# Kernel optimization log

Measured on AMD Instinct MI355X. Metric: run time of the kernel, lower is better.

The kernel has to match this reference:

```python
import jax, jax.numpy as jnp
import numpy as np

KSIZE = 3   # patch kernel
NSIZE = 7   # search neighborhood
SCALE = 4   # downscale factor
ALPHA = 1


def _patches(x, k, pad_mode):
    # x: [b,c,h,w] -> [b, c*k*k, h, w], feature ordering channel-major
    # (matches torch.nn.functional.unfold ordering).
    if pad_mode == 'reflect':
        p = k // 2
        xp = jnp.pad(x, ((0, 0), (0, 0), (p, p), (p, p)), mode='reflect')
        return jax.lax.conv_general_dilated_patches(xp, (k, k), (1, 1), 'VALID')
    return jax.lax.conv_general_dilated_patches(x, (k, k), (1, 1), 'SAME')


def census(x):
    # UFlow-style soft census transform (the CensusTransform used in this repo):
    # grayscale*255, 3x3 zero-padded patches minus center, soft-sign normalize.
    gray = (0.299 * x[:, 0:1] + 0.587 * x[:, 1:2] + 0.114 * x[:, 2:3]) * 255.0
    p = _patches(gray, KSIZE, 'zero')          # [b, 9, h, w]
    t = p - gray
    return t / jnp.sqrt(0.81 + t * t)


def downsample(x):
    b, c, h, w = x.shape
    return jax.image.resize(x, (b, c, h // SCALE, w // SCALE), method='cubic')


def unfold_center(x):
    # _unfold(data, with_unfold=False): [b,c,h,w] -> [b, hw, c*k*k]
    x = downsample(x)
    b, c, h, w = x.shape
    p = _patches(x, KSIZE, 'reflect').reshape(b, c * KSIZE * KSIZE, h * w)
    return p.transpose(0, 2, 1)


def unfold_nbr(x):
    # _unfold(data, with_unfold=True): [b,c,h,w] -> [b, hw, n*n, c*k*k]
    x = downsample(x)
    b, c, h, w = x.shape
    d1 = _patches(x, KSIZE, 'reflect')          # [b, c*k*k, h, w]
    c1 = d1.shape[1]
    d2 = _patches(d1, NSIZE, 'reflect')         # [b, c1*n*n, h, w]
    d2 = d2.reshape(b, c1, NSIZE * NSIZE, h * w)
    return d2.transpose(0, 3, 2, 1)


def reference(pred, I):
    # --- census-space distance + argmin over 2*n*n candidates ---
    p_ct = unfold_center(census(pred))                       # [b, hw, 81]
    nbr_ct = jnp.concatenate(
        [unfold_nbr(census(I[:, 0])), unfold_nbr(census(I[:, 1]))], axis=2
    )                                                        # [b, hw, 2n^2, 81]
    # ||p - n||^2 expanded as p2 + n2 - 2 p.n (avoids the huge repeated diff)
    p2 = jnp.sum(p_ct * p_ct, axis=-1)                       # [b, hw]
    n2 = jnp.sum(nbr_ct * nbr_ct, axis=-1)                   # [b, hw, 2n^2]
    dis = p2[:, :, None] + n2 - 2.0 * jnp.einsum('bpc,bpnc->bpn', p_ct, nbr_ct)
    ind = jnp.argmin(dis, axis=2)                            # [b, hw]
    # --- gather matched raw patches and compute loss ---
    p = unfold_center(pred)                                  # [b, hw, 27]
    nbr = jnp.concatenate(
        [unfold_nbr(I[:, 0]), unfold_nbr(I[:, 1])], axis=2
    )                                                        # [b, hw, 2n^2, 27]
    matched = jnp.take_along_axis(nbr, ind[:, :, None, None], axis=2)[:, :, 0]
    return jnp.mean((p - matched) ** 2 * 0.5)


def setup_inputs() -> dict:
    key = jax.random.key(0)
    k1, k2 = jax.random.split(key)
    pred = jax.random.normal(k1, (2, 3, 384, 384), dtype=jnp.float32)
    I = jax.random.normal(k2, (2, 2, 3, 384, 384), dtype=jnp.float32)
    return {'pred': pred, 'I': I}
```

## Files before the change

kernel.cpp:

```cpp
#include <hip/hip_runtime.h>
#include <math.h>

#define FH 384
#define FW 384
#define DH 96
#define DW 96
#define NIMG 6
#define PLANE (DH * DW)
#define NPIX (2 * PLANE)

__device__ __forceinline__ float keysc(float x) {
    if (x < 1.f) return ((1.5f * x - 2.5f) * x) * x + 1.f;
    if (x < 2.f) return ((-0.5f * x + 2.5f) * x - 4.f) * x + 2.f;
    return 0.f;
}

__device__ __forceinline__ int refl(int i, int n) {
    if (i < 0) i = -i;
    if (i >= n) i = 2 * (n - 1) - i;
    return i;
}

__global__ void k_field(const float* __restrict__ pred, const float* __restrict__ I,
                        float* __restrict__ CF) {
    int idx = blockIdx.x * 256 + threadIdx.x;
    const int total = NIMG * FH * FW;
    if (idx >= total) return;
    int x   = idx % FW;
    int t1  = idx / FW;
    int r   = t1 % FH;
    int img = t1 / FH;
    const float* src;
    if (img < 2) {
        src = pred + img * 3 * FH * FW;
    } else {
        int j = (img - 2) >> 1, b = (img - 2) & 1;
        src = I + ((b * 2 + j) * 3) * FH * FW;
    }
    const int planeF = FH * FW;
    auto grayAt = [&](int rr, int cc) -> float {
        const float* s = src + rr * FW + cc;
        return (0.299f * s[0] + 0.587f * s[planeF] + 0.114f * s[2 * planeF]) * 255.0f;
    };
    float gc = grayAt(r, x);
    float* out = CF + ((size_t)img * 8) * planeF + r * FW + x;
    int ck = 0;
#pragma unroll
    for (int k = 0; k < 9; ++k) {
        if (k == 4) continue;
        int dy = k / 3 - 1, dx = k % 3 - 1;
        int r2 = r + dy, c2 = x + dx;
        float gn = (r2 < 0 || r2 >= FH || c2 < 0 || c2 >= FW) ? 0.f : grayAt(r2, c2);
        float tt = gn - gc;
        out[ck * planeF] = tt / sqrtf(0.81f + tt * tt);
        ++ck;
    }
}

#define CTOT (NIMG * 9 * DH * (FW / 4))
#define RTOT (NIMG * 3 * DH * (FW / 4))
__global__ void k_downH(const float* __restrict__ CF, const float* __restrict__ pred,
                        const float* __restrict__ I, float* __restrict__ CH,
                        float* __restrict__ RH) {
    int idx = blockIdx.x * 256 + threadIdx.x;
    if (idx >= CTOT + RTOT) return;
    const int planeF = FH * FW;

    const float4* F;
    float4* outp;
    int yo;
    bool zero_out = false;
    if (idx < CTOT) {
        int x4 = idx % 96;
        int t1 = idx / 96;
        yo     = t1 % DH;
        int t2 = t1 / DH;
        int k  = t2 % 9;
        int img = t2 / 9;
        outp = (float4*)CH + idx;
        if (k == 4) {
            zero_out = true;
            F = (const float4*)CF;
        } else {
            int ck = (k < 4) ? k : k - 1;
            F = (const float4*)(CF + (size_t)(img * 8 + ck) * planeF) + x4;
        }
    } else {
        int rid = idx - CTOT;
        int x4 = rid % 96;
        int t1 = rid / 96;
        yo     = t1 % DH;
        int t2 = t1 / DH;
        int c  = t2 % 3;
        int img = t2 / 3;
        const float* src;
        if (img < 2) {
            src = pred + (img * 3 + c) * planeF;
        } else {
            int j = (img - 2) >> 1, b = (img - 2) & 1;
            src = I + (((b * 2 + j) * 3) + c) * planeF;
        }
        F = (const float4*)src + x4;
        outp = (float4*)RH + rid;
    }

    if (zero_out) {
        *outp = make_float4(0.f, 0.f, 0.f, 0.f);
        return;
    }

    int rbase = 4 * yo - 6;
    float4 acc = make_float4(0.f, 0.f, 0.f, 0.f);
    float z = 0.f;
    if (rbase >= 0 && rbase + 15 < FH) {
#pragma unroll
        for (int t = 0; t < 16; ++t) {
            float w = keysc(fabsf((float)t - 7.5f) * 0.25f);
            z += w;
            float4 v = F[(rbase + t) * 96];
            acc.x += w * v.x; acc.y += w * v.y; acc.z += w * v.z; acc.w += w * v.w;
        }
    } else {
#pragma unroll
        for (int t = 0; t < 16; ++t) {
            int r = rbase + t;
            if (r < 0 || r >= FH) continue;
            float w = keysc(fabsf((float)t - 7.5f) * 0.25f);
            z += w;
            float4 v = F[r * 96];
            acc.x += w * v.x; acc.y += w * v.y; acc.z += w * v.z; acc.w += w * v.w;
        }
    }
    *outp = make_float4(acc.x / z, acc.y / z, acc.z / z, acc.w / z);
}

__global__ void k_downW(const float* __restrict__ src, float* __restrict__ dst, int nrows) {
    int idx = blockIdx.x * 256 + threadIdx.x;
    int total = nrows * DW;
    if (idx >= total) return;
    int xo = idx % DW;
    int row = idx / DW;
    const float* s = src + row * FW;
    float acc = 0.f, z = 0.f;
#pragma unroll
    for (int t = 0; t < 16; ++t) {
        int i = 4 * xo - 6 + t;
        if (i < 0 || i >= FW) continue;
        float w = keysc(fabsf((float)t - 7.5f) * 0.25f);
        z += w;
        acc += w * s[i];
    }
    dst[idx] = acc / z;
}

__global__ void k_n2(const float* __restrict__ CD, float* __restrict__ N2) {
    int idx = blockIdx.x * 256 + threadIdx.x;
    if (idx >= 4 * PLANE) return;
    int img4 = idx / PLANE;
    int pos  = idx % PLANE;
    int y = pos / DW, x = pos % DW;
    int ry[3], rx[3];
#pragma unroll
    for (int kk = 0; kk < 3; ++kk) {
        ry[kk] = refl(y + kk - 1, DH);
        rx[kk] = refl(x + kk - 1, DW);
    }
    const float* C = CD + (2 + img4) * 9 * PLANE;
    float s = 0.f;
#pragma unroll
    for (int c = 0; c < 9; ++c)
#pragma unroll
        for (int ky = 0; ky < 3; ++ky)
#pragma unroll
            for (int kx = 0; kx < 3; ++kx) {
                float v = C[c * PLANE + ry[ky] * DW + rx[kx]];
                s += v * v;
            }
    N2[idx] = s;
}

__global__ __launch_bounds__(256) void k_match_int(const float* __restrict__ CD,
                                                   const float* __restrict__ N2,
                                                   float* __restrict__ bestd,
                                                   int* __restrict__ bestn) {
    int bid  = blockIdx.x;
    int g    = bid / 72;
    int tile = bid % 72;
    int pid  = tile * 256 + threadIdx.x;
    int j  = g / 7;
    int dy = g % 7 - 3;
    int b   = pid / PLANE;
    int pos = pid % PLANE;
    int y = pos / DW, x = pos % DW;

    int yy = refl(y + dy, DH);
    int r0 = refl(yy - 1, DH), r1 = yy, r2 = refl(yy + 1, DH);
    int pr0 = refl(y - 1, DH), pr2 = refl(y + 1, DH);
    int xb = min(max(x - 4, 0), DW - 9);
    int xp = min(max(x - 1, 0), DW - 3);

    const float* Cp  = CD + (b * 9) * PLANE;
    const float* Cn  = CD + ((2 + 2 * j + b) * 9) * PLANE;
    const float* N2p = N2 + (2 * j + b) * PLANE;

    float dot[7];
#pragma unroll
    for (int i = 0; i < 7; ++i) dot[i] = 0.f;

#pragma unroll
    for (int c = 0; c < 9; ++c) {
        const float* pc = Cp + c * PLANE;
        const float* nc = Cn + c * PLANE;
        float p0[3], p1[3], p2[3];
#pragma unroll
        for (int kx = 0; kx < 3; ++kx) {
            p0[kx] = pc[pr0 * DW + xp + kx];
            p1[kx] = pc[y   * DW + xp + kx];
            p2[kx] = pc[pr2 * DW + xp + kx];
        }
        float w0[9], w1[9], w2[9];
#pragma unroll
        for (int i = 0; i < 9; ++i) {
            w0[i] = nc[r0 * DW + xb + i];
            w1[i] = nc[r1 * DW + xb + i];
            w2[i] = nc[r2 * DW + xb + i];
        }
#pragma unroll
        for (int dx = 0; dx < 7; ++dx) {
            float d = dot[dx];
            d += p0[0] * w0[dx + 0]; d += p0[1] * w0[dx + 1]; d += p0[2] * w0[dx + 2];
            d += p1[0] * w1[dx + 0]; d += p1[1] * w1[dx + 1]; d += p1[2] * w1[dx + 2];
            d += p2[0] * w2[dx + 0]; d += p2[1] * w2[dx + 1]; d += p2[2] * w2[dx + 2];
            dot[dx] = d;
        }
    }

    float best = INFINITY;
    int bn = 1 << 30;
    int nbase = j * 49 + (dy + 3) * 7;
#pragma unroll
    for (int dx = 0; dx < 7; ++dx) {
        int xxc = min(max(x + dx - 3, 0), DW - 1);
        float dis = N2p[yy * DW + xxc] - 2.f * dot[dx];
        if (dis < best) { best = dis; bn = nbase + dx; }
    }
    if (x >= 4 && x < 92) {
        bestd[g * NPIX + pid] = best;
        bestn[g * NPIX + pid] = bn;
    }
}

__global__ __launch_bounds__(256) void k_match_edge(const float* __restrict__ CD,
                                                    const float* __restrict__ N2,
                                                    float* __restrict__ bestd,
                                                    int* __restrict__ bestn) {
    __shared__ float part[4][64];
    __shared__ float disw[4][8];

    int wid  = threadIdx.x >> 6;
    int lane = threadIdx.x & 63;
    int item = blockIdx.x * 4 + wid;
    int g  = item / 1536;
    int pe = item % 1536;
    int j = g / 7, dy = g % 7 - 3;
    int b   = pe / 768;
    int rem = pe % 768;
    int y  = rem / 8;
    int xi = rem % 8;
    int x  = (xi < 4) ? xi : 88 + xi;
    int pid = b * PLANE + y * DW + x;
    int yy = refl(y + dy, DH);

    int c = lane / 7, dx = lane % 7;
    float partial = 0.f;
    if (lane < 63) {
        int xx = refl(x + dx - 3, DW);
        const float* pc = CD + (b * 9 + c) * PLANE;
        const float* nc = CD + ((2 + 2 * j + b) * 9 + c) * PLANE;
#pragma unroll
        for (int ky = 0; ky < 3; ++ky) {
            int pry = refl(y + ky - 1, DH);
            int nry = refl(yy + ky - 1, DH);
#pragma unroll
            for (int kx = 0; kx < 3; ++kx) {
                int prx = refl(x + kx - 1, DW);
                int nrx = refl(xx + kx - 1, DW);
                partial += pc[pry * DW + prx] * nc[nry * DW + nrx];
            }
        }
    }
    part[wid][lane] = partial;
    __syncthreads();

    if (lane < 7) {
        float dot = 0.f;
#pragma unroll
        for (int cc = 0; cc < 9; ++cc) dot += part[wid][cc * 7 + lane];
        int xxl = refl(x + lane - 3, DW);
        disw[wid][lane] = N2[(2 * j + b) * PLANE + yy * DW + xxl] - 2.f * dot;
    }
    __syncthreads();

    if (lane == 0) {
        float best = INFINITY;
        int bn = 1 << 30;
        int nbase = j * 49 + (dy + 3) * 7;
#pragma unroll
        for (int dxx = 0; dxx < 7; ++dxx) {
            float d = disw[wid][dxx];
            if (d < best) { best = d; bn = nbase + dxx; }
        }
        bestd[g * NPIX + pid] = best;
        bestn[g * NPIX + pid] = bn;
    }
}

__global__ __launch_bounds__(256) void k_combine(const float* __restrict__ bestd,
                                                 const int* __restrict__ bestn,
                                                 const float* __restrict__ RD,
                                                 float* __restrict__ partial) {
    int pid = blockIdx.x * 256 + threadIdx.x;
    int b   = pid / PLANE;
    int pos = pid % PLANE;
    int y = pos / DW, x = pos % DW;

    float d0 = bestd[pid];
    int   n0 = bestn[pid];
#pragma unroll
    for (int g = 1; g < 14; ++g) {
        float d = bestd[g * NPIX + pid];
        int   n = bestn[g * NPIX + pid];
        if (d < d0 || (d == d0 && n < n0)) { d0 = d; n0 = n; }
    }

    int j = n0 / 49, rr = n0 % 49;
    int dy = rr / 7 - 3, dx = rr % 7 - 3;
    int yy = refl(y + dy, DH), xx = refl(x + dx, DW);
    int ry0[3], rx0[3], ry[3], rx[3];
#pragma unroll
    for (int kk = 0; kk < 3; ++kk) {
        ry0[kk] = refl(y + kk - 1, DH);
        rx0[kk] = refl(x + kk - 1, DW);
        ry[kk]  = refl(yy + kk - 1, DH);
        rx[kk]  = refl(xx + kk - 1, DW);
    }
    const float* RDp = RD + b * 3 * PLANE;
    const float* RDn = RD + (2 + 2 * j + b) * 3 * PLANE;
    float loss = 0.f;
#pragma unroll
    for (int c = 0; c < 3; ++c)
#pragma unroll
        for (int ky = 0; ky < 3; ++ky)
#pragma unroll
            for (int kx = 0; kx < 3; ++kx) {
                float a = RDp[c * PLANE + ry0[ky] * DW + rx0[kx]];
                float m = RDn[c * PLANE + ry[ky] * DW + rx[kx]];
                float d = a - m;
                loss += d * d;
            }

    __shared__ float red[256];
    red[threadIdx.x] = loss;
    __syncthreads();
#pragma unroll
    for (int s = 128; s > 0; s >>= 1) {
        if (threadIdx.x < s) red[threadIdx.x] += red[threadIdx.x + s];
        __syncthreads();
    }
    if (threadIdx.x == 0) partial[blockIdx.x] = red[0];
}

#define NPART 72
__global__ void k_final(const float* __restrict__ partial, float* __restrict__ out) {
    __shared__ float red[128];
    float v = (threadIdx.x < NPART) ? partial[threadIdx.x] : 0.f;
    red[threadIdx.x] = v;
    __syncthreads();
#pragma unroll
    for (int s = 64; s > 0; s >>= 1) {
        if (threadIdx.x < s) red[threadIdx.x] += red[threadIdx.x + s];
        __syncthreads();
    }
    if (threadIdx.x == 0) out[0] = red[0] * (0.5f / 497664.0f);
}

extern "C" void kernel_launch(void* const* d_in, const int* in_sizes, int n_in,
                              void* d_out, int out_size, void* d_ws, size_t ws_size,
                              hipStream_t stream) {
    const float* pred = (const float*)d_in[0];
    const float* I    = (const float*)d_in[1];
    float* out = (float*)d_out;
    float* ws  = (float*)d_ws;

    float* CD   = ws;
    float* RD   = CD + 497664;
    float* S    = RD + 165888;
    float* CF   = S;
    float* CH   = S + 7077888;
    float* RH   = S + 9068544;
    float* N2   = S;
    float* bestd = S + 36864;
    int*   bestn = (int*)(S + 294912);
    float* part  = S + 552960;

    k_field<<<(NIMG * FH * FW + 255) / 256, 256, 0, stream>>>(pred, I, CF);
    k_downH<<<(CTOT + RTOT + 255) / 256, 256, 0, stream>>>(CF, pred, I, CH, RH);
    k_downW<<<((NIMG * 12 * DH) * DW + 255) / 256, 256, 0, stream>>>(CH, CD, NIMG * 12 * DH);
    k_n2<<<(4 * PLANE + 255) / 256, 256, 0, stream>>>(CD, N2);
    k_match_int<<<14 * 72, 256, 0, stream>>>(CD, N2, bestd, bestn);
    k_match_edge<<<(14 * 1536) / 4, 256, 0, stream>>>(CD, N2, bestd, bestn);
    k_combine<<<NPIX / 256, 256, 0, stream>>>(bestd, bestn, RD, part);
    k_final<<<1, 128, 0, stream>>>(part, out);
}
```

Baseline: 121.0 us.

## Fuse census transform with vertical downsample via shared memory and fold final reduction

Replaces the full-resolution census field kernel and the separate vertical cubic-downsample kernel with one tiled kernel. Each block computes grayscale into shared memory, builds each census channel tile in shared memory and immediately filters it vertically, so the large full-resolution census field is never written to or read back from global memory. Separately, the final reduction kernel is removed by having the last k_combine block, detected through an atomic counter that k_n2 resets, sum the partial results. This costs extra shared memory and per-channel barriers, and recomputes some rows because the tiles overlap.

Result: slower. 135.4 us (+11.9%).

```diff
diff --git a/kernel.cpp b/kernel.cpp
--- a/kernel.cpp
+++ b/kernel.cpp
@@ -21,75 +21,88 @@
     return i;
 }
 
-__global__ void k_field(const float* __restrict__ pred, const float* __restrict__ I,
-                        float* __restrict__ CF) {
-    int idx = blockIdx.x * 256 + threadIdx.x;
-    const int total = NIMG * FH * FW;
-    if (idx >= total) return;
-    int x   = idx % FW;
-    int t1  = idx / FW;
-    int r   = t1 % FH;
-    int img = t1 / FH;
-    const float* src;
-    if (img < 2) {
-        src = pred + img * 3 * FH * FW;
+#define CBLK 432
+#define RTOT (NIMG * 3 * DH * (FW / 4))
+__global__ __launch_bounds__(256) void k_census_raw(const float* __restrict__ pred,
+                                                    const float* __restrict__ I,
+                                                    float* __restrict__ CH,
+                                                    float* __restrict__ RH) {
+    __shared__ float gsh[30][130];
+    __shared__ float fsh[28][128];
+    const int planeF = FH * FW;
+    int tid = threadIdx.x;
+
+    if (blockIdx.x < CBLK) {
+        int bid = blockIdx.x;
+        int img = bid / 72;
+        int rem = bid % 72;
+        int ys  = rem / 3;
+        int xt  = rem % 3;
+        int yo0 = ys * 4;
+        int x0  = xt * 128;
+        int r0g = 4 * yo0 - 7;
+        int r0f = 4 * yo0 - 6;
+
+        const float* src;
+        if (img < 2) {
+            src = pred + img * 3 * planeF;
+        } else {
+            int j = (img - 2) >> 1, b = (img - 2) & 1;
+            src = I + ((b * 2 + j) * 3) * planeF;
+        }
+
+        for (int i = tid; i < 30 * 130; i += 256) {
+            int rr = i / 130, cc = i % 130;
+            int ra = r0g + rr, ca = x0 - 1 + cc;
+            float v = 0.f;
+            if (ra >= 0 && ra < FH && ca >= 0 && ca < FW) {
+                const float* s = src + ra * FW + ca;
+                v = (0.299f * s[0] + 0.587f * s[planeF] + 0.114f * s[2 * planeF]) * 255.0f;
+            }
+            gsh[rr][cc] = v;
+        }
+        __syncthreads();
+
+        for (int o = tid; o < 512; o += 256) {
+            int q = o >> 7, xl = o & 127;
+            CH[((img * 9 + 4) * DH + yo0 + q) * FW + x0 + xl] = 0.f;
+        }
+
+        for (int k = 0; k < 9; ++k) {
+            if (k == 4) continue;
+            int dy = k / 3 - 1, dx = k % 3 - 1;
+            for (int i = tid; i < 28 * 128; i += 256) {
+                int fr = i >> 7, fc = i & 127;
+                int ra = r0f + fr, ca = x0 + fc;
+                float gc = gsh[fr + 1][fc + 1];
+                int r2 = ra + dy, c2 = ca + dx;
+                float gn = (r2 < 0 || r2 >= FH || c2 < 0 || c2 >= FW)
+                               ? 0.f : gsh[fr + 1 + dy][fc + 1 + dx];
+                float tt = gn - gc;
+                fsh[fr][fc] = tt / sqrtf(0.81f + tt * tt);
+            }
+            __syncthreads();
+            for (int o = tid; o < 512; o += 256) {
+                int q = o >> 7, xl = o & 127;
+                int yo = yo0 + q;
+                float acc = 0.f, z = 0.f;
+#pragma unroll
+                for (int t = 0; t < 16; ++t) {
+                    int r = 4 * yo - 6 + t;
+                    if (r < 0 || r >= FH) continue;
+                    float w = keysc(fabsf((float)t - 7.5f) * 0.25f);
+                    z += w;
+                    acc += w * fsh[4 * q + t][xl];
+                }
+                CH[((img * 9 + k) * DH + yo) * FW + x0 + xl] = acc / z;
+            }
+            __syncthreads();
+        }
     } else {
-        int j = (img - 2) >> 1, b = (img - 2) & 1;
-        src = I + ((b * 2 + j) * 3) * FH * FW;
-    }
-    const int planeF = FH * FW;
-    auto grayAt = [&](int rr, int cc) -> float {
-        const float* s = src + rr * FW + cc;
-        return (0.299f * s[0] + 0.587f * s[planeF] + 0.114f * s[2 * planeF]) * 255.0f;
-    };
-    float gc = grayAt(r, x);
-    float* out = CF + ((size_t)img * 8) * planeF + r * FW + x;
-    int ck = 0;
-#pragma unroll
-    for (int k = 0; k < 9; ++k) {
-        if (k == 4) continue;
-        int dy = k / 3 - 1, dx = k % 3 - 1;
-        int r2 = r + dy, c2 = x + dx;
-        float gn = (r2 < 0 || r2 >= FH || c2 < 0 || c2 >= FW) ? 0.f : grayAt(r2, c2);
-        float tt = gn - gc;
-        out[ck * planeF] = tt / sqrtf(0.81f + tt * tt);
-        ++ck;
-    }
-}
-
-#define CTOT (NIMG * 9 * DH * (FW / 4))
-#define RTOT (NIMG * 3 * DH * (FW / 4))
-__global__ void k_downH(const float* __restrict__ CF, const float* __restrict__ pred,
-                        const float* __restrict__ I, float* __restrict__ CH,
-                        float* __restrict__ RH) {
-    int idx = blockIdx.x * 256 + threadIdx.x;
-    if (idx >= CTOT + RTOT) return;
-    const int planeF = FH * FW;
-
-    const float4* F;
-    float4* outp;
-    int yo;
-    bool zero_out = false;
-    if (idx < CTOT) {
-        int x4 = idx % 96;
-        int t1 = idx / 96;
-        yo     = t1 % DH;
-        int t2 = t1 / DH;
-        int k  = t2 % 9;
-        int img = t2 / 9;
-        outp = (float4*)CH + idx;
-        if (k == 4) {
-            zero_out = true;
-            F = (const float4*)CF;
-        } else {
-            int ck = (k < 4) ? k : k - 1;
-            F = (const float4*)(CF + (size_t)(img * 8 + ck) * planeF) + x4;
-        }
-    } else {
-        int rid = idx - CTOT;
+        int rid = (blockIdx.x - CBLK) * 256 + tid;
         int x4 = rid % 96;
         int t1 = rid / 96;
-        yo     = t1 % DH;
+        int yo = t1 % DH;
         int t2 = t1 / DH;
         int c  = t2 % 3;
         int img = t2 / 3;
@@ -100,38 +113,31 @@
             int j = (img - 2) >> 1, b = (img - 2) & 1;
             src = I + (((b * 2 + j) * 3) + c) * planeF;
         }
-        F = (const float4*)src + x4;
-        outp = (float4*)RH + rid;
-    }
-
-    if (zero_out) {
-        *outp = make_float4(0.f, 0.f, 0.f, 0.f);
-        return;
-    }
-
-    int rbase = 4 * yo - 6;
-    float4 acc = make_float4(0.f, 0.f, 0.f, 0.f);
-    float z = 0.f;
-    if (rbase >= 0 && rbase + 15 < FH) {
-#pragma unroll
-        for (int t = 0; t < 16; ++t) {
-            float w = keysc(fabsf((float)t - 7.5f) * 0.25f);
-            z += w;
-            float4 v = F[(rbase + t) * 96];
-            acc.x += w * v.x; acc.y += w * v.y; acc.z += w * v.z; acc.w += w * v.w;
-        }
-    } else {
-#pragma unroll
-        for (int t = 0; t < 16; ++t) {
-            int r = rbase + t;
-            if (r < 0 || r >= FH) continue;
-            float w = keysc(fabsf((float)t - 7.5f) * 0.25f);
-            z += w;
-            float4 v = F[r * 96];
-            acc.x += w * v.x; acc.y += w * v.y; acc.z += w * v.z; acc.w += w * v.w;
-        }
-    }
-    *outp = make_float4(acc.x / z, acc.y / z, acc.z / z, acc.w / z);
+        const float4* F = (const float4*)src + x4;
+        int rbase = 4 * yo - 6;
+        float4 acc = make_float4(0.f, 0.f, 0.f, 0.f);
+        float z = 0.f;
+        if (rbase >= 0 && rbase + 15 < FH) {
+#pragma unroll
+            for (int t = 0; t < 16; ++t) {
+                float w = keysc(fabsf((float)t - 7.5f) * 0.25f);
+                z += w;
+                float4 v = F[(rbase + t) * 96];
+                acc.x += w * v.x; acc.y += w * v.y; acc.z += w * v.z; acc.w += w * v.w;
+            }
+        } else {
+#pragma unroll
+            for (int t = 0; t < 16; ++t) {
+                int r = rbase + t;
+                if (r < 0 || r >= FH) continue;
+                float w = keysc(fabsf((float)t - 7.5f) * 0.25f);
+                z += w;
+                float4 v = F[r * 96];
+                acc.x += w * v.x; acc.y += w * v.y; acc.z += w * v.z; acc.w += w * v.w;
+            }
+        }
+        ((float4*)RH)[rid] = make_float4(acc.x / z, acc.y / z, acc.z / z, acc.w / z);
+    }
 }
 
 __global__ void k_downW(const float* __restrict__ src, float* __restrict__ dst, int nrows) {
@@ -153,8 +159,10 @@
     dst[idx] = acc / z;
 }
 
-__global__ void k_n2(const float* __restrict__ CD, float* __restrict__ N2) {
+__global__ void k_n2(const float* __restrict__ CD, float* __restrict__ N2,
+                     int* __restrict__ counter) {
     int idx = blockIdx.x * 256 + threadIdx.x;
+    if (idx == 0) *counter = 0;
     if (idx >= 4 * PLANE) return;
     int img4 = idx / PLANE;
     int pos  = idx % PLANE;
@@ -315,10 +323,13 @@
     }
 }
 
+#define NPART 72
 __global__ __launch_bounds__(256) void k_combine(const float* __restrict__ bestd,
                                                  const int* __restrict__ bestn,
                                                  const float* __restrict__ RD,
-                                                 float* __restrict__ partial) {
+                                                 float* __restrict__ partial,
+                                                 int* __restrict__ counter,
+                                                 float* __restrict__ out) {
     int pid = blockIdx.x * 256 + threadIdx.x;
     int b   = pid / PLANE;
     int pos = pid % PLANE;
@@ -360,6 +371,7 @@
             }
 
     __shared__ float red[256];
+    __shared__ int sdone;
     red[threadIdx.x] = loss;
     __syncthreads();
 #pragma unroll
@@ -367,21 +379,32 @@
         if (threadIdx.x < s) red[threadIdx.x] += red[threadIdx.x + s];
         __syncthreads();
     }
-    if (threadIdx.x == 0) partial[blockIdx.x] = red[0];
-}
-
-#define NPART 72
-__global__ void k_final(const float* __restrict__ partial, float* __restrict__ out) {
-    __shared__ float red[128];
-    float v = (threadIdx.x < NPART) ? partial[threadIdx.x] : 0.f;
-    red[threadIdx.x] = v;
+    if (threadIdx.x == 0) {
+        __hip_atomic_store(&partial[blockIdx.x], red[0], __ATOMIC_RELEASE,
+                           __HIP_MEMORY_SCOPE_AGENT);
+        int prev = __hip_atomic_fetch_add(counter, 1, __ATOMIC_ACQ_REL,
+                                          __HIP_MEMORY_SCOPE_AGENT);
+        sdone = (prev == NPART - 1);
+    }
     __syncthreads();
-#pragma unroll
-    for (int s = 64; s > 0; s >>= 1) {
-        if (threadIdx.x < s) red[threadIdx.x] += red[threadIdx.x + s];
+
+    if (sdone) {
+        __shared__ float red2[128];
+        if (threadIdx.x < 128) {
+            float v = (threadIdx.x < NPART)
+                ? __hip_atomic_load(&partial[threadIdx.x], __ATOMIC_ACQUIRE,
+                                    __HIP_MEMORY_SCOPE_AGENT)
+                : 0.f;
+            red2[threadIdx.x] = v;
+        }
         __syncthreads();
-    }
-    if (threadIdx.x == 0) out[0] = red[0] * (0.5f / 497664.0f);
+#pragma unroll
+        for (int s = 64; s > 0; s >>= 1) {
+            if (threadIdx.x < s) red2[threadIdx.x] += red2[threadIdx.x + s];
+            __syncthreads();
+        }
+        if (threadIdx.x == 0) out[0] = red2[0] * (0.5f / 497664.0f);
+    }
 }
 
 extern "C" void kernel_launch(void* const* d_in, const int* in_sizes, int n_in,
@@ -395,20 +418,18 @@
     float* CD   = ws;
     float* RD   = CD + 497664;
     float* S    = RD + 165888;
-    float* CF   = S;
-    float* CH   = S + 7077888;
-    float* RH   = S + 9068544;
+    float* CH   = S;
+    float* RH   = S + 1990656;
     float* N2   = S;
     float* bestd = S + 36864;
     int*   bestn = (int*)(S + 294912);
     float* part  = S + 552960;
-
-    k_field<<<(NIMG * FH * FW + 255) / 256, 256, 0, stream>>>(pred, I, CF);
-    k_downH<<<(CTOT + RTOT + 255) / 256, 256, 0, stream>>>(CF, pred, I, CH, RH);
+    int*   counter = (int*)(S + 553032);
+
+    k_census_raw<<<CBLK + RTOT / 256, 256, 0, stream>>>(pred, I, CH, RH);
     k_downW<<<((NIMG * 12 * DH) * DW + 255) / 256, 256, 0, stream>>>(CH, CD, NIMG * 12 * DH);
-    k_n2<<<(4 * PLANE + 255) / 256, 256, 0, stream>>>(CD, N2);
+    k_n2<<<(4 * PLANE + 255) / 256, 256, 0, stream>>>(CD, N2, counter);
     k_match_int<<<14 * 72, 256, 0, stream>>>(CD, N2, bestd, bestn);
     k_match_edge<<<(14 * 1536) / 4, 256, 0, stream>>>(CD, N2, bestd, bestn);
-    k_combine<<<NPIX / 256, 256, 0, stream>>>(bestd, bestn, RD, part);
-    k_final<<<1, 128, 0, stream>>>(part, out);
-}
+    k_combine<<<NPIX / 256, 256, 0, stream>>>(bestd, bestn, RD, part, counter, out);
+}
```
